# Optimization experiments

Hardware: AMD Instinct MI355X
Metric: run time of the kernel (lower is better)

The kernel has to match this reference:

```python
import jax, jax.numpy as jnp
import numpy as np

# solver hyperparameters (from init_kwargs)
N_LEVELS = 4
N_PRE = 2
N_POST = 2
N_COARSE = 20
OMEGA = 0.9
N_CYCLES = 2
LAM = 1.0
DX0 = 1.0
FINE_N = 2048


def _apply_operator(u, mask, cx, cy, dx2, dy2):
    """A u = div(c grad u) - lambda*u, 5-point masked stencil, zero-padded ghosts."""
    u_m = u * mask
    u_e = jnp.zeros_like(u_m).at[:, :-1].set(u_m[:, 1:])
    u_w = jnp.zeros_like(u_m).at[:, 1:].set(u_m[:, :-1])
    u_n = jnp.zeros_like(u_m).at[:-1, :].set(u_m[1:, :])
    u_s = jnp.zeros_like(u_m).at[1:, :].set(u_m[:-1, :])
    cx_w = jnp.zeros_like(cx).at[:, 1:].set(cx[:, :-1])
    cy_s = jnp.zeros_like(cy).at[1:, :].set(cy[:-1, :])
    lap = (cx * (u_e - u_m) - cx_w * (u_m - u_w)) / dx2 \
        + (cy * (u_n - u_m) - cy_s * (u_m - u_s)) / dy2
    return (lap - LAM * u_m) * mask


def _inv_diagonal(mask, cx, cy, dx2, dy2):
    cx_w = jnp.zeros_like(cx).at[:, 1:].set(cx[:, :-1])
    cy_s = jnp.zeros_like(cy).at[1:, :].set(cy[:-1, :])
    diag = -((cx + cx_w) / dx2 + (cy + cy_s) / dy2) - LAM
    return jnp.where(diag != 0, 1.0 / diag, 0.0) * mask


def _weighted_jacobi(u, rhs, mask, cx, cy, inv_diag, dx2, dy2, n_iters):
    def _step(_, u_cur):
        r = rhs - _apply_operator(u_cur, mask, cx, cy, dx2, dy2)
        return (u_cur + OMEGA * inv_diag * r) * mask
    return jax.lax.fori_loop(0, n_iters, _step, u)


def _restrict(v, mask_fine, mask_coarse):
    v_m = v * mask_fine
    sum4 = v_m[::2, ::2] + v_m[1::2, ::2] + v_m[::2, 1::2] + v_m[1::2, 1::2]
    count = mask_fine[::2, ::2] + mask_fine[1::2, ::2] + mask_fine[::2, 1::2] + mask_fine[1::2, 1::2]
    return sum4 / jnp.maximum(count, 1.0) * mask_coarse


def _prolongate(v_coarse, mask_coarse, mask_fine):
    ny_c, nx_c = v_coarse.shape
    ny_f, nx_f = 2 * ny_c, 2 * nx_c
    vp = jnp.pad(v_coarse * mask_coarse, ((1, 1), (1, 1)))
    mp = jnp.pad(mask_coarse, ((1, 1), (1, 1)))
    vc = vp[1:-1, 1:-1]
    mc = mp[1:-1, 1:-1]

    def _interp(dj, di):
        sj, si = 2 * dj - 1, 2 * di - 1
        v_si = vp[1:-1, 1 + si:nx_c + 1 + si]
        m_si = mp[1:-1, 1 + si:nx_c + 1 + si]
        v_sj = vp[1 + sj:ny_c + 1 + sj, 1:-1]
        m_sj = mp[1 + sj:ny_c + 1 + sj, 1:-1]
        v_d = vp[1 + sj:ny_c + 1 + sj, 1 + si:nx_c + 1 + si]
        m_d = mp[1 + sj:ny_c + 1 + sj, 1 + si:nx_c + 1 + si]
        w = 9 * vc + 3 * v_si + 3 * v_sj + v_d
        d = 9 * mc + 3 * m_si + 3 * m_sj + m_d
        return w / jnp.maximum(d, 1.0)

    v_fine = jnp.zeros((ny_f, nx_f), dtype=v_coarse.dtype)
    v_fine = v_fine.at[::2, ::2].set(_interp(0, 0))
    v_fine = v_fine.at[::2, 1::2].set(_interp(0, 1))
    v_fine = v_fine.at[1::2, ::2].set(_interp(1, 0))
    v_fine = v_fine.at[1::2, 1::2].set(_interp(1, 1))
    return v_fine * mask_fine


def setup_inputs() -> dict:
    key = jax.random.key(0)
    ks = jax.random.split(key, 1 + 2 * N_LEVELS)
    inp = {}
    n = FINE_N
    for l in range(N_LEVELS):
        mask = jnp.ones((n, n), dtype=jnp.float32)
        cx = jax.random.uniform(ks[1 + 2 * l], (n, n), jnp.float32) + 0.5
        cy = jax.random.uniform(ks[2 + 2 * l], (n, n), jnp.float32) + 0.5
        cx = cx.at[:, -1].set(0.0)  # zero-flux boundary faces
        cy = cy.at[-1, :].set(0.0)
        inp[f'mask{l}'] = mask
        inp[f'cx{l}'] = cx
        inp[f'cy{l}'] = cy
        n //= 2
    inp['rhs'] = jax.random.normal(ks[0], (FINE_N, FINE_N), jnp.float32)
    return inp


def _solve(rhs, masks, cxs, cys):
    levels = []
    for l in range(N_LEVELS):
        dx2 = (DX0 * (2 ** l)) ** 2
        inv = _inv_diagonal(masks[l], cxs[l], cys[l], dx2, dx2)
        levels.append((masks[l], cxs[l], cys[l], inv, dx2, dx2))

    def vcycle(u, r, lvl):
        mask, cx, cy, inv, dx2, dy2 = levels[lvl]
        u = _weighted_jacobi(u, r, mask, cx, cy, inv, dx2, dy2, N_PRE)
        if lvl == N_LEVELS - 1:
            return _weighted_jacobi(u, r, mask, cx, cy, inv, dx2, dy2, N_COARSE)
        res = (r - _apply_operator(u, mask, cx, cy, dx2, dy2)) * mask
        r_c = _restrict(res, mask, levels[lvl + 1][0])
        e_c = vcycle(jnp.zeros_like(r_c), r_c, lvl + 1)
        u = u + _prolongate(e_c, levels[lvl + 1][0], mask)
        return _weighted_jacobi(u, r, mask, cx, cy, inv, dx2, dy2, N_POST)

    u = jnp.zeros_like(rhs)
    for _ in range(N_CYCLES):
        u = vcycle(u, rhs, 0)
    return u


def reference(rhs, mask0, mask1, mask2, mask3, cx0, cx1, cx2, cx3, cy0, cy1, cy2, cy3):
    return _solve(rhs, [mask0, mask1, mask2, mask3], [cx0, cx1, cx2, cx3], [cy0, cy1, cy2, cy3])
```

## Files before the change

kernel.cpp:

```cpp
#include <hip/hip_runtime.h>


namespace {

constexpr float OMEGA_C = 0.9f;

template<int STEPS, int RG, int BLK, bool U0, bool RESTRICT, bool PROLONG>
__global__ __launch_bounds__(BLK) void mg_fused(
    const float* __restrict__ uin, float* __restrict__ uout,
    const float* __restrict__ rhs,
    const float* __restrict__ cx, const float* __restrict__ cy,
    float inv_dx2, int n,
    const float* __restrict__ e,
    float* __restrict__ rc)
{
    constexpr int H    = STEPS + (RESTRICT ? 1 : 0);
    constexpr int TT   = RG - 2 * H;
    constexpr int NS   = BLK / RG;
    constexpr int SR   = RG / NS;
    constexpr int SROW = RG + 2;
    static_assert(TT > 0 && BLK % RG == 0 && RG % NS == 0, "geometry");
    static_assert(!RESTRICT || (TT % 2 == 0), "restrict needs even tile");

    __shared__ float sA[RG * SROW];
    __shared__ float sB[RG * SROW];

    const int tid = threadIdx.x;
    const int tx  = tid & (RG - 1);
    const int ty  = tid / RG;
    const int jb  = ty * SR;
    const int bx  = blockIdx.x * TT - H;
    const int by  = blockIdx.y * TT - H;
    const int gi  = bx + tx;
    const int nc  = n >> 1;
    const int gj0 = by + jb;

    float u[SR], rh[SR], sv[SR], cxs[SR], cxw[SR], cyn[SR];
    float cys0;

    if (tid < RG) {
        sA[tid * SROW] = 0.0f;  sA[tid * SROW + RG + 1] = 0.0f;
        sB[tid * SROW] = 0.0f;  sB[tid * SROW + RG + 1] = 0.0f;
    }

    const bool interior = (bx >= 2) && (by >= 2) &&
                          (bx + RG + 2 <= n) && (by + RG + 2 <= n);

    if (interior) {
        const size_t g0 = (size_t)gj0 * n + gi;
        cys0 = cy[g0 - n] * inv_dx2;
#pragma unroll
        for (int k = 0; k < SR; ++k) {
            const size_t g = g0 + (size_t)k * n;
            cxs[k] = cx[g] * inv_dx2;
            cyn[k] = cy[g] * inv_dx2;
            rh[k]  = rhs[g];
            float vu;
            if constexpr (U0) vu = 0.0f; else vu = uin[g];
            if constexpr (PROLONG) {
                const int gj = gj0 + k;
                const int ic = gi >> 1, jc = gj >> 1;
                const int ii = ic + ((gi & 1) ? 1 : -1);
                const int jj = jc + ((gj & 1) ? 1 : -1);
                const float vc  = e[jc * nc + ic];
                const float vsi = e[jc * nc + ii];
                const float vsj = e[jj * nc + ic];
                const float vd  = e[jj * nc + ii];
                vu += (((9.0f * vc + 3.0f * vsi) + 3.0f * vsj) + vd) * 0.0625f;
            }
            u[k] = vu;
        }
    } else {
        const bool gi_ok = (unsigned)gi < (unsigned)n;
        {
            const int gjm = gj0 - 1;
            const bool okm = gi_ok && ((unsigned)gjm < (unsigned)n);
            cys0 = okm ? cy[(size_t)gjm * n + gi] * inv_dx2 : 0.0f;
        }
#pragma unroll
        for (int k = 0; k < SR; ++k) {
            const int gj = gj0 + k;
            const bool ok = gi_ok && ((unsigned)gj < (unsigned)n);
            float vcx = 0.f, vcy = 0.f, vrh = 0.f, vu = 0.f;
            if (ok) {
                const size_t g = (size_t)gj * n + gi;
                vcx = cx[g] * inv_dx2;
                vcy = cy[g] * inv_dx2;
                vrh = rhs[g];
                if constexpr (!U0) vu = uin[g];
                if constexpr (PROLONG) {
                    const int ic = gi >> 1, jc = gj >> 1;
                    const int ii = ic + ((gi & 1) ? 1 : -1);
                    const int jj = jc + ((gj & 1) ? 1 : -1);
                    const bool iok = (unsigned)ii < (unsigned)nc;
                    const bool jok = (unsigned)jj < (unsigned)nc;
                    const float vc  = e[jc * nc + ic];
                    const float vsi = iok ? e[jc * nc + ii] : 0.0f;
                    const float vsj = jok ? e[jj * nc + ic] : 0.0f;
                    const float vd  = (iok && jok) ? e[jj * nc + ii] : 0.0f;
                    const float ws  = ((9.0f * vc + 3.0f * vsi) + 3.0f * vsj) + vd;
                    const float dn  = ((9.0f + (iok ? 3.0f : 0.0f)) + (jok ? 3.0f : 0.0f))
                                    + ((iok && jok) ? 1.0f : 0.0f);
                    vu += ws / dn;
                }
            }
            cxs[k] = vcx; cyn[k] = vcy; rh[k] = vrh; u[k] = vu;
        }
    }

#pragma unroll
    for (int k = 0; k < SR; ++k) cxw[k] = __shfl_up(cxs[k], 1, RG);

#pragma unroll
    for (int k = 0; k < SR; ++k) {
        const float cys  = k ? cyn[k - 1] : cys0;
        const float diag = -((cxs[k] + cxw[k]) + (cyn[k] + cys)) - 1.0f;
        const float inv  = (diag != 0.0f) ? 1.0f / diag : 0.0f;
        sv[k] = OMEGA_C * inv;
    }

    {
        const int base = jb * SROW + 1 + tx;
#pragma unroll
        for (int k = 0; k < SR; ++k) sA[base + k * SROW] = u[k];
    }
    __syncthreads();

    float* cur = sA;
    float* nxt = sB;
    for (int s = 0; s < STEPS; ++s) {
        const float us_edge = (jb > 0)       ? cur[(jb - 1)  * SROW + 1 + tx] : 0.0f;
        const float un_edge = (jb + SR < RG) ? cur[(jb + SR) * SROW + 1 + tx] : 0.0f;
        const int base = jb * SROW + 1 + tx;
        float prev_old = us_edge;
        const bool last = (s == STEPS - 1);
#pragma unroll
        for (int k = 0; k < SR; ++k) {
            const float um = u[k];
            const float ue = cur[base + k * SROW + 1];
            const float uw = cur[base + k * SROW - 1];
            const float un = (k < SR - 1) ? u[k + 1] : un_edge;
            const float us = prev_old;
            const float cys = k ? cyn[k - 1] : cys0;
            const float lx = cxs[k] * (ue - um) - cxw[k] * (um - uw);
            const float ly = cyn[k] * (un - um) - cys    * (um - us);
            const float r  = rh[k] - ((lx + ly) - um);
            prev_old = um;
            u[k] = um + sv[k] * r;
        }
        if (last && !RESTRICT) break;
#pragma unroll
        for (int k = 0; k < SR; ++k) nxt[base + k * SROW] = u[k];
        __syncthreads();
        float* t = cur; cur = nxt; nxt = t;
    }

#pragma unroll
    for (int k = 0; k < SR; ++k) {
        const int lr = jb + k;
        const int gj = by + lr;
        if (lr >= H && lr < H + TT && tx >= H && tx < H + TT &&
            (interior || (gj < n && gi < n))) {
            uout[(size_t)gj * n + gi] = u[k];
        }
    }

    if constexpr (RESTRICT) {
        float res[SR];
        const float us_edge = (jb > 0)       ? cur[(jb - 1)  * SROW + 1 + tx] : 0.0f;
        const float un_edge = (jb + SR < RG) ? cur[(jb + SR) * SROW + 1 + tx] : 0.0f;
        const int base = jb * SROW + 1 + tx;
        float prev_old = us_edge;
#pragma unroll
        for (int k = 0; k < SR; ++k) {
            const float um = u[k];
            const float ue = cur[base + k * SROW + 1];
            const float uw = cur[base + k * SROW - 1];
            const float un = (k < SR - 1) ? u[k + 1] : un_edge;
            const float us = prev_old;
            const float cys = k ? cyn[k - 1] : cys0;
            const float lx = cxs[k] * (ue - um) - cxw[k] * (um - uw);
            const float ly = cyn[k] * (un - um) - cys    * (um - us);
            res[k] = rh[k] - ((lx + ly) - um);
            prev_old = um;
        }
        __syncthreads();
#pragma unroll
        for (int k = 0; k < SR; ++k) nxt[base + k * SROW] = res[k];
        __syncthreads();

        constexpr int TC = TT / 2;
        for (int t = tid; t < TC * TC; t += BLK) {
            const int tj = t / TC, ti = t - tj * TC;
            const int a = (H + 2 * tj) * SROW + 1 + (H + 2 * ti);
            const float sum = ((nxt[a] + nxt[a + SROW]) + nxt[a + 1]) + nxt[a + SROW + 1];
            const int gjc = blockIdx.y * TC + tj;
            const int gic = blockIdx.x * TC + ti;
            if (gjc < nc && gic < nc) rc[gjc * nc + gic] = sum * 0.25f;
        }
    }
}

static dim3 grd(int n, int tt) { int g = (n + tt - 1) / tt; return dim3(g, g); }

}

extern "C" void kernel_launch(void* const* d_in, const int* in_sizes, int n_in,
                              void* d_out, int out_size, void* d_ws, size_t ws_size,
                              hipStream_t stream) {
    (void)in_sizes; (void)n_in; (void)out_size; (void)ws_size;

    const float* cx0 = (const float*)d_in[1];
    const float* cy0 = (const float*)d_in[2];
    const float* cx1 = (const float*)d_in[4];
    const float* cy1 = (const float*)d_in[5];
    const float* cx2 = (const float*)d_in[7];
    const float* cy2 = (const float*)d_in[8];
    const float* cx3 = (const float*)d_in[10];
    const float* cy3 = (const float*)d_in[11];
    const float* rhs = (const float*)d_in[12];

    float* O = (float*)d_out;
    float* w = (float*)d_ws;
    float* W   = w; w += 2048 * 2048;
    float* rc1 = w; w += 1024 * 1024;
    float* a1  = w; w += 1024 * 1024;
    float* b1  = w; w += 1024 * 1024;
    float* rc2 = w; w += 512 * 512;
    float* a2  = w; w += 512 * 512;
    float* b2  = w; w += 512 * 512;
    float* rc3 = w; w += 256 * 256;
    float* a3  = w; w += 256 * 256;
    float* b3  = w; w += 256 * 256;

    const dim3 blk(256, 1, 1);

    mg_fused<2, 32, 256, true, true, false><<<grd(2048, 26), blk, 0, stream>>>(
        nullptr, O, rhs, cx0, cy0, 1.0f, 2048, nullptr, rc1);
    mg_fused<2, 32, 256, true, true, false><<<grd(1024, 26), blk, 0, stream>>>(
        nullptr, a1, rc1, cx1, cy1, 0.25f, 1024, nullptr, rc2);
    mg_fused<2, 32, 256, true, true, false><<<grd(512, 26), blk, 0, stream>>>(
        nullptr, a2, rc2, cx2, cy2, 0.0625f, 512, nullptr, rc3);
    mg_fused<11, 32, 256, true,  false, false><<<grd(256, 10), blk, 0, stream>>>(
        nullptr, a3, rc3, cx3, cy3, 0.015625f, 256, nullptr, nullptr);
    mg_fused<11, 32, 256, false, false, false><<<grd(256, 10), blk, 0, stream>>>(
        a3, b3, rc3, cx3, cy3, 0.015625f, 256, nullptr, nullptr);
    mg_fused<2, 32, 256, false, false, true><<<grd(512, 28), blk, 0, stream>>>(
        a2, b2, rc2, cx2, cy2, 0.0625f, 512, b3, nullptr);
    mg_fused<2, 32, 256, false, false, true><<<grd(1024, 28), blk, 0, stream>>>(
        a1, b1, rc1, cx1, cy1, 0.25f, 1024, b2, nullptr);
    mg_fused<4, 32, 256, false, true, true><<<grd(2048, 22), blk, 0, stream>>>(
        O, W, rhs, cx0, cy0, 1.0f, 2048, b1, rc1);
    mg_fused<2, 32, 256, true, true, false><<<grd(1024, 26), blk, 0, stream>>>(
        nullptr, a1, rc1, cx1, cy1, 0.25f, 1024, nullptr, rc2);
    mg_fused<2, 32, 256, true, true, false><<<grd(512, 26), blk, 0, stream>>>(
        nullptr, a2, rc2, cx2, cy2, 0.0625f, 512, nullptr, rc3);
    mg_fused<11, 32, 256, true,  false, false><<<grd(256, 10), blk, 0, stream>>>(
        nullptr, a3, rc3, cx3, cy3, 0.015625f, 256, nullptr, nullptr);
    mg_fused<11, 32, 256, false, false, false><<<grd(256, 10), blk, 0, stream>>>(
        a3, b3, rc3, cx3, cy3, 0.015625f, 256, nullptr, nullptr);
    mg_fused<2, 32, 256, false, false, true><<<grd(512, 28), blk, 0, stream>>>(
        a2, b2, rc2, cx2, cy2, 0.0625f, 512, b3, nullptr);
    mg_fused<2, 32, 256, false, false, true><<<grd(1024, 28), blk, 0, stream>>>(
        a1, b1, rc1, cx1, cy1, 0.25f, 1024, b2, nullptr);
    mg_fused<2, 32, 256, false, false, true><<<grd(2048, 28), blk, 0, stream>>>(
        W, O, rhs, cx0, cy0, 1.0f, 2048, b1, nullptr);
}
```

Before: 317.6 us.

## Use rectangular 64x32 tiles on fine level and XCD-aware block swizzle

Generalizes the fused multigrid kernel to rectangular tiles and runs the 2048 level with 64-wide x 32-tall regions, reducing halo overlap and redundant stencil work per useful cell. Flattens the grid to 1D and remaps block IDs so that contiguous tiles are assigned to the same XCD, improving L2 locality of neighbouring tiles. Wider tiles raise per-thread register use (8 rows per thread) and shared memory, which may lower occupancy.

```diff
diff --git a/kernel.cpp b/kernel.cpp
--- a/kernel.cpp
+++ b/kernel.cpp
@@ -5,32 +5,42 @@
 
 constexpr float OMEGA_C = 0.9f;
 
-template<int STEPS, int RG, int BLK, bool U0, bool RESTRICT, bool PROLONG>
-__global__ __launch_bounds__(BLK) void mg_fused(
+template<int STEPS, int RGX, int RGY, bool U0, bool RESTRICT, bool PROLONG>
+__global__ __launch_bounds__(256) void mg_fused(
     const float* __restrict__ uin, float* __restrict__ uout,
     const float* __restrict__ rhs,
     const float* __restrict__ cx, const float* __restrict__ cy,
-    float inv_dx2, int n,
+    float inv_dx2, int n, int gx,
     const float* __restrict__ e,
     float* __restrict__ rc)
 {
+    constexpr int BLK  = 256;
     constexpr int H    = STEPS + (RESTRICT ? 1 : 0);
-    constexpr int TT   = RG - 2 * H;
-    constexpr int NS   = BLK / RG;
-    constexpr int SR   = RG / NS;
-    constexpr int SROW = RG + 2;
-    static_assert(TT > 0 && BLK % RG == 0 && RG % NS == 0, "geometry");
-    static_assert(!RESTRICT || (TT % 2 == 0), "restrict needs even tile");
-
-    __shared__ float sA[RG * SROW];
-    __shared__ float sB[RG * SROW];
+    constexpr int TTX  = RGX - 2 * H;
+    constexpr int TTY  = RGY - 2 * H;
+    constexpr int NSY  = BLK / RGX;
+    constexpr int SR   = RGY / NSY;
+    constexpr int SROW = RGX + 2;
+    static_assert(TTX > 0 && TTY > 0 && BLK % RGX == 0 && RGY % NSY == 0, "geometry");
+    static_assert(!RESTRICT || (TTX % 2 == 0 && TTY % 2 == 0), "restrict tile even");
+
+    __shared__ float sA[RGY * SROW];
+    __shared__ float sB[RGY * SROW];
+
+    const int nwg  = gridDim.x;
+    const int bid  = blockIdx.x;
+    const int q    = nwg >> 3, r = nwg & 7;
+    const int xcd  = bid & 7;
+    const int wgid = (xcd < r ? xcd * (q + 1) : r * (q + 1) + (xcd - r) * q) + (bid >> 3);
+    const int tiley = wgid / gx;
+    const int tilex = wgid - tiley * gx;
 
     const int tid = threadIdx.x;
-    const int tx  = tid & (RG - 1);
-    const int ty  = tid / RG;
+    const int tx  = tid & (RGX - 1);
+    const int ty  = tid / RGX;
     const int jb  = ty * SR;
-    const int bx  = blockIdx.x * TT - H;
-    const int by  = blockIdx.y * TT - H;
+    const int bx  = tilex * TTX - H;
+    const int by  = tiley * TTY - H;
     const int gi  = bx + tx;
     const int nc  = n >> 1;
     const int gj0 = by + jb;
@@ -38,13 +48,13 @@
     float u[SR], rh[SR], sv[SR], cxs[SR], cxw[SR], cyn[SR];
     float cys0;
 
-    if (tid < RG) {
-        sA[tid * SROW] = 0.0f;  sA[tid * SROW + RG + 1] = 0.0f;
-        sB[tid * SROW] = 0.0f;  sB[tid * SROW + RG + 1] = 0.0f;
+    if (tid < RGY) {
+        sA[tid * SROW] = 0.0f;  sA[tid * SROW + RGX + 1] = 0.0f;
+        sB[tid * SROW] = 0.0f;  sB[tid * SROW + RGX + 1] = 0.0f;
     }
 
     const bool interior = (bx >= 2) && (by >= 2) &&
-                          (bx + RG + 2 <= n) && (by + RG + 2 <= n);
+                          (bx + RGX + 2 <= n) && (by + RGY + 2 <= n);
 
     if (interior) {
         const size_t g0 = (size_t)gj0 * n + gi;
@@ -109,7 +119,7 @@
     }
 
 #pragma unroll
-    for (int k = 0; k < SR; ++k) cxw[k] = __shfl_up(cxs[k], 1, RG);
+    for (int k = 0; k < SR; ++k) cxw[k] = __shfl_up(cxs[k], 1, RGX);
 
 #pragma unroll
     for (int k = 0; k < SR; ++k) {
@@ -129,8 +139,8 @@
     float* cur = sA;
     float* nxt = sB;
     for (int s = 0; s < STEPS; ++s) {
-        const float us_edge = (jb > 0)       ? cur[(jb - 1)  * SROW + 1 + tx] : 0.0f;
-        const float un_edge = (jb + SR < RG) ? cur[(jb + SR) * SROW + 1 + tx] : 0.0f;
+        const float us_edge = (jb > 0)        ? cur[(jb - 1)  * SROW + 1 + tx] : 0.0f;
+        const float un_edge = (jb + SR < RGY) ? cur[(jb + SR) * SROW + 1 + tx] : 0.0f;
         const int base = jb * SROW + 1 + tx;
         float prev_old = us_edge;
         const bool last = (s == STEPS - 1);
@@ -159,7 +169,7 @@
     for (int k = 0; k < SR; ++k) {
         const int lr = jb + k;
         const int gj = by + lr;
-        if (lr >= H && lr < H + TT && tx >= H && tx < H + TT &&
+        if (lr >= H && lr < H + TTY && tx >= H && tx < H + TTX &&
             (interior || (gj < n && gi < n))) {
             uout[(size_t)gj * n + gi] = u[k];
         }
@@ -167,8 +177,8 @@
 
     if constexpr (RESTRICT) {
         float res[SR];
-        const float us_edge = (jb > 0)       ? cur[(jb - 1)  * SROW + 1 + tx] : 0.0f;
-        const float un_edge = (jb + SR < RG) ? cur[(jb + SR) * SROW + 1 + tx] : 0.0f;
+        const float us_edge = (jb > 0)        ? cur[(jb - 1)  * SROW + 1 + tx] : 0.0f;
+        const float un_edge = (jb + SR < RGY) ? cur[(jb + SR) * SROW + 1 + tx] : 0.0f;
         const int base = jb * SROW + 1 + tx;
         float prev_old = us_edge;
 #pragma unroll
@@ -189,19 +199,20 @@
         for (int k = 0; k < SR; ++k) nxt[base + k * SROW] = res[k];
         __syncthreads();
 
-        constexpr int TC = TT / 2;
-        for (int t = tid; t < TC * TC; t += BLK) {
-            const int tj = t / TC, ti = t - tj * TC;
+        constexpr int TCX = TTX / 2;
+        constexpr int TCY = TTY / 2;
+        for (int t = tid; t < TCX * TCY; t += BLK) {
+            const int tj = t / TCX, ti = t - tj * TCX;
             const int a = (H + 2 * tj) * SROW + 1 + (H + 2 * ti);
             const float sum = ((nxt[a] + nxt[a + SROW]) + nxt[a + 1]) + nxt[a + SROW + 1];
-            const int gjc = blockIdx.y * TC + tj;
-            const int gic = blockIdx.x * TC + ti;
+            const int gjc = tiley * TCY + tj;
+            const int gic = tilex * TCX + ti;
             if (gjc < nc && gic < nc) rc[gjc * nc + gic] = sum * 0.25f;
         }
     }
 }
 
-static dim3 grd(int n, int tt) { int g = (n + tt - 1) / tt; return dim3(g, g); }
+static inline int cdiv(int a, int b) { return (a + b - 1) / b; }
 
 }
 
@@ -235,34 +246,34 @@
 
     const dim3 blk(256, 1, 1);
 
-    mg_fused<2, 32, 256, true, true, false><<<grd(2048, 26), blk, 0, stream>>>(
-        nullptr, O, rhs, cx0, cy0, 1.0f, 2048, nullptr, rc1);
-    mg_fused<2, 32, 256, true, true, false><<<grd(1024, 26), blk, 0, stream>>>(
-        nullptr, a1, rc1, cx1, cy1, 0.25f, 1024, nullptr, rc2);
-    mg_fused<2, 32, 256, true, true, false><<<grd(512, 26), blk, 0, stream>>>(
-        nullptr, a2, rc2, cx2, cy2, 0.0625f, 512, nullptr, rc3);
-    mg_fused<11, 32, 256, true,  false, false><<<grd(256, 10), blk, 0, stream>>>(
-        nullptr, a3, rc3, cx3, cy3, 0.015625f, 256, nullptr, nullptr);
-    mg_fused<11, 32, 256, false, false, false><<<grd(256, 10), blk, 0, stream>>>(
-        a3, b3, rc3, cx3, cy3, 0.015625f, 256, nullptr, nullptr);
-    mg_fused<2, 32, 256, false, false, true><<<grd(512, 28), blk, 0, stream>>>(
-        a2, b2, rc2, cx2, cy2, 0.0625f, 512, b3, nullptr);
-    mg_fused<2, 32, 256, false, false, true><<<grd(1024, 28), blk, 0, stream>>>(
-        a1, b1, rc1, cx1, cy1, 0.25f, 1024, b2, nullptr);
-    mg_fused<4, 32, 256, false, true, true><<<grd(2048, 22), blk, 0, stream>>>(
-        O, W, rhs, cx0, cy0, 1.0f, 2048, b1, rc1);
-    mg_fused<2, 32, 256, true, true, false><<<grd(1024, 26), blk, 0, stream>>>(
-        nullptr, a1, rc1, cx1, cy1, 0.25f, 1024, nullptr, rc2);
-    mg_fused<2, 32, 256, true, true, false><<<grd(512, 26), blk, 0, stream>>>(
-        nullptr, a2, rc2, cx2, cy2, 0.0625f, 512, nullptr, rc3);
-    mg_fused<11, 32, 256, true,  false, false><<<grd(256, 10), blk, 0, stream>>>(
-        nullptr, a3, rc3, cx3, cy3, 0.015625f, 256, nullptr, nullptr);
-    mg_fused<11, 32, 256, false, false, false><<<grd(256, 10), blk, 0, stream>>>(
-        a3, b3, rc3, cx3, cy3, 0.015625f, 256, nullptr, nullptr);
-    mg_fused<2, 32, 256, false, false, true><<<grd(512, 28), blk, 0, stream>>>(
-        a2, b2, rc2, cx2, cy2, 0.0625f, 512, b3, nullptr);
-    mg_fused<2, 32, 256, false, false, true><<<grd(1024, 28), blk, 0, stream>>>(
-        a1, b1, rc1, cx1, cy1, 0.25f, 1024, b2, nullptr);
-    mg_fused<2, 32, 256, false, false, true><<<grd(2048, 28), blk, 0, stream>>>(
-        W, O, rhs, cx0, cy0, 1.0f, 2048, b1, nullptr);
+    const int gxA0 = cdiv(2048, 58), gyA0 = cdiv(2048, 26);
+    const int gxX  = cdiv(2048, 54), gyX  = cdiv(2048, 22);
+    const int gxB0 = cdiv(2048, 60), gyB0 = cdiv(2048, 28);
+    const int gxA1 = cdiv(1024, 26), gxB1 = cdiv(1024, 28);
+    const int gxA2 = cdiv(512, 26),  gxB2 = cdiv(512, 28);
+    const int gxC  = cdiv(256, 10);
+
+    for (int c = 0; c < 2; ++c) {
+        if (c == 0) {
+            mg_fused<2, 64, 32, true, true, false><<<dim3(gxA0 * gyA0), blk, 0, stream>>>(
+                nullptr, O, rhs, cx0, cy0, 1.0f, 2048, gxA0, nullptr, rc1);
+        } else {
+            mg_fused<4, 64, 32, false, true, true><<<dim3(gxX * gyX), blk, 0, stream>>>(
+                O, W, rhs, cx0, cy0, 1.0f, 2048, gxX, b1, rc1);
+        }
+        mg_fused<2, 32, 32, true, true, false><<<dim3(gxA1 * gxA1), blk, 0, stream>>>(
+            nullptr, a1, rc1, cx1, cy1, 0.25f, 1024, gxA1, nullptr, rc2);
+        mg_fused<2, 32, 32, true, true, false><<<dim3(gxA2 * gxA2), blk, 0, stream>>>(
+            nullptr, a2, rc2, cx2, cy2, 0.0625f, 512, gxA2, nullptr, rc3);
+        mg_fused<11, 32, 32, true,  false, false><<<dim3(gxC * gxC), blk, 0, stream>>>(
+            nullptr, a3, rc3, cx3, cy3, 0.015625f, 256, gxC, nullptr, nullptr);
+        mg_fused<11, 32, 32, false, false, false><<<dim3(gxC * gxC), blk, 0, stream>>>(
+            a3, b3, rc3, cx3, cy3, 0.015625f, 256, gxC, nullptr, nullptr);
+        mg_fused<2, 32, 32, false, false, true><<<dim3(gxB2 * gxB2), blk, 0, stream>>>(
+            a2, b2, rc2, cx2, cy2, 0.0625f, 512, gxB2, b3, nullptr);
+        mg_fused<2, 32, 32, false, false, true><<<dim3(gxB1 * gxB1), blk, 0, stream>>>(
+            a1, b1, rc1, cx1, cy1, 0.25f, 1024, gxB1, b2, nullptr);
+    }
+    mg_fused<2, 64, 32, false, false, true><<<dim3(gxB0 * gyB0), blk, 0, stream>>>(
+        W, O, rhs, cx0, cy0, 1.0f, 2048, gxB0, b1, nullptr);
 }
```

Result: faster. 262.6 us (-17.3%).
